# Performance work log

Hardware: AMD Instinct MI355X
Metric: run time of the kernel (lower is better)

Reference implementation:

```python
import jax, jax.numpy as jnp
import numpy as np


def setup_inputs() -> dict:
    key = jax.random.key(0)
    k1, k2 = jax.random.split(key)
    out = jax.random.uniform(k1, (32, 128, 128, 9, 5), dtype=jnp.float32)
    target = jax.random.uniform(k2, (32, 128, 128, 3, 6), dtype=jnp.float32)
    return {"out": out, "target": target}


def _loss(out, target):
    # out: [B, GX, GY, A, 5], target: [B, GX, GY, Q, 6]
    B, GX, GY, Q, _ = target.shape
    A = out.shape[3]
    # the original loop breaks after qub == 0, so only the first gt per cell is used
    st = target[:, :, :, 0, :]            # [B, GX, GY, 6]
    pos = st[..., 5] > 0.8                # [B, GX, GY] positive-cell mask

    dtype = out.dtype
    # grid-cell centers zxdwx / zxdwy
    zx = (jnp.arange(GX, dtype=dtype) / GX + 1.0 / (2 * GX))[None, :, None, None]
    zy = (jnp.arange(GY, dtype=dtype) / GY + 1.0 / (2 * GY))[None, None, :, None]

    # gt box (center format) -> corners; broadcast over anchor dim
    acx = st[..., 0][..., None]
    acy = st[..., 1][..., None]
    aw = st[..., 2][..., None]
    ah = st[..., 3][..., None]
    ax1, ay1, ax2, ay2 = acx - aw / 2, acy - ah / 2, acx + aw / 2, acy + ah / 2

    # predicted box: offsets decoded relative to grid cell
    bcx = out[..., 0] - 0.5 + zx
    bcy = out[..., 1] - 0.5 + zy
    bw = out[..., 2] - 0.5 + 1.0 / GX
    bh = out[..., 3] - 0.5 + 1.0 / GY
    bx1, by1, bx2, by2 = bcx - bw / 2, bcy - bh / 2, bcx + bw / 2, bcy + bh / 2

    # IoU (intersection zeroed when either overlap extent <= 0)
    iw = jnp.minimum(ax2, bx2) - jnp.maximum(ax1, bx1)
    ih = jnp.minimum(ay2, by2) - jnp.maximum(ay1, by1)
    cross = jnp.where((iw > 0) & (ih > 0), iw * ih, 0.0)
    area_a = (ax2 - ax1) * (ay2 - ay1)
    area_b = (bx2 - bx1) * (by2 - by1)
    union = area_a + area_b - cross
    iou = cross / (union + 1e-6)

    # DIoU term: center distance over bound-box diagonal
    d = jnp.sqrt(((bx1 + bx2) / 2 - (ax1 + ax2) / 2) ** 2
                 + ((by1 + by2) / 2 - (ay1 + ay2) / 2) ** 2)
    cx1 = jnp.minimum(ax1, bx1)
    cy1 = jnp.minimum(ay1, by1)
    cx2 = jnp.maximum(ax2, bx2)
    cy2 = jnp.maximum(ay2, by2)
    c = jnp.sqrt((cx2 - cx1) ** 2 + (cy2 - cy1) ** 2)
    diou = iou - d ** 2 / c ** 2

    # CIoU aspect-ratio term
    v = (4.0 / np.pi ** 2) * (jnp.arctan((ax2 - ax1) / (ay2 - ay1))
                              - jnp.arctan((bx2 - bx1) / (by2 - by1))) ** 2
    alpha = v / (1 - iou + v)
    los = 1 - (diou - alpha * v)      # [B, GX, GY, A]

    obj = out[..., 4]
    posA = pos[..., None]             # broadcast mask over anchors

    jsq = (jnp.sum(pos) * A).astype(dtype)
    qit = (jnp.sum(~pos) * A).astype(dtype)
    allloss = jnp.sum(jnp.where(posA, los + (1 - obj), 0.0))
    jbb = jnp.sum(jnp.where(posA, iou, 0.0))
    huhuh = jnp.sum(jnp.where(posA, 1 - obj, 0.0))
    zsd = jnp.sum(jnp.where(posA, (1 - obj) ** 2, obj ** 2))

    return (allloss / jsq + zsd / (jsq + qit), jbb / jsq, huhuh / jsq)


def reference(out, target):
    return _loss(out, target)
```

## Files before the change

kernel.cpp:

```cpp
#include <hip/hip_runtime.h>
#include <math.h>

constexpr int kGX     = 128;
constexpr int kGY     = 128;
constexpr int kA      = 9;
constexpr int kNCells = 32 * kGX * kGY;
constexpr int kN      = kNCells * kA;

constexpr int kGroups        = kN / 4;
constexpr int kTiles         = kGroups / 256;
constexpr int kTilesPerBlock = 2;
constexpr int kBlocks        = kTiles / kTilesPerBlock;
static_assert(kBlocks * kTilesPerBlock * 256 * 4 == kN, "exact cover");

__device__ inline float frcp(float x) { return __builtin_amdgcn_rcpf(x); }

__device__ inline float fast_atan(float r) {
    const float x = fabsf(r);
    const bool inv = x > 1.f;
    const float t = inv ? frcp(x) : x;
    const float t2 = t * t;
    float p = fmaf(t2, 0.0208351f, -0.0851330f);
    p = fmaf(t2, p, 0.1801410f);
    p = fmaf(t2, p, -0.3302995f);
    p = fmaf(t2, p, 0.9998660f);
    p = t * p;
    float res = inv ? (1.5707963f - p) : p;
    return r < 0.f ? -res : res;
}

struct Rec {
    float ax1, ax2, ay1, ay2, acx, acy, area, atg, zx, zy, posf;
};

__device__ inline Rec make_rec(const float* __restrict__ tgt, int cell) {
    const float2* t2p = (const float2*)(tgt + (size_t)cell * 18);
    const float2 a01 = t2p[0];
    const float2 a23 = t2p[1];
    const float conf = ((const float*)t2p)[5];
    Rec r;
    r.acx = a01.x; r.acy = a01.y;
    r.ax1 = a01.x - 0.5f * a23.x; r.ax2 = a01.x + 0.5f * a23.x;
    r.ay1 = a01.y - 0.5f * a23.y; r.ay2 = a01.y + 0.5f * a23.y;
    r.area = a23.x * a23.y;
    r.atg  = fast_atan(a23.x * frcp(a23.y));
    const int gy = cell & (kGY - 1);
    const int gx = (cell >> 7) & (kGX - 1);
    r.zx = (float)gx * (1.f / kGX) + 0.5f / kGX;
    r.zy = (float)gy * (1.f / kGY) + 0.5f / kGY;
    r.posf = (conf > 0.8f) ? 1.f : 0.f;
    return r;
}

__global__ __launch_bounds__(256)
void loss_main(const float* __restrict__ outp, const float* __restrict__ tgt,
               double* __restrict__ acc, int mode) {
    __shared__ float4 sbuf[1280];

    const int tid = threadIdx.x;
    float t_jsq = 0.f, t_all = 0.f, t_jbb = 0.f, t_huh = 0.f, t_zsd = 0.f;

    for (int tt = 0; tt < kTilesPerBlock; ++tt) {
        const int tile = blockIdx.x * kTilesPerBlock + tt;
        const int gid  = tile * 256 + tid;
        const int a0   = gid * 4;

        const int cell0 = (int)(__umulhi((unsigned)a0, 0x38E38E39u) >> 1);
        const int r0    = a0 - cell0 * 9;
        const int cell1 = min(cell0 + 1, kNCells - 1);
        const Rec RA = make_rec(tgt, cell0);
        const Rec RB = make_rec(tgt, cell1);

        if (tt) __syncthreads();
        const float4* src = (const float4*)outp + (size_t)tile * 1280;
        #pragma unroll
        for (int k = 0; k < 5; ++k) sbuf[k * 256 + tid] = src[k * 256 + tid];
        __syncthreads();

        const float* so = (const float*)sbuf + tid * 20;
        const float4 q0 = *(const float4*)(so +  0);
        const float4 q1 = *(const float4*)(so +  4);
        const float4 q2 = *(const float4*)(so +  8);
        const float4 q3 = *(const float4*)(so + 12);
        const float4 q4 = *(const float4*)(so + 16);

        const float o[20] = {q0.x, q0.y, q0.z, q0.w, q1.x, q1.y, q1.z, q1.w,
                             q2.x, q2.y, q2.z, q2.w, q3.x, q3.y, q3.z, q3.w,
                             q4.x, q4.y, q4.z, q4.w};

        #pragma unroll
        for (int j = 0; j < 4; ++j) {
            const bool cross = (r0 + j) >= 9;
            const float ax1 = cross ? RB.ax1 : RA.ax1, ax2 = cross ? RB.ax2 : RA.ax2;
            const float ay1 = cross ? RB.ay1 : RA.ay1, ay2 = cross ? RB.ay2 : RA.ay2;
            const float acx = cross ? RB.acx : RA.acx, acy = cross ? RB.acy : RA.acy;
            const float area_a = cross ? RB.area : RA.area;
            const float atan_a = cross ? RB.atg : RA.atg;
            const float zx = cross ? RB.zx : RA.zx, zy = cross ? RB.zy : RA.zy;
            const float posf = cross ? RB.posf : RA.posf;
            const bool pos = posf > 0.5f;

            const float o0 = o[j * 5 + 0], o1 = o[j * 5 + 1], o2 = o[j * 5 + 2];
            const float o3 = o[j * 5 + 3], obj = o[j * 5 + 4];

            const float bcx = o0 - 0.5f + zx;
            const float bcy = o1 - 0.5f + zy;
            const float bw  = o2 - 0.5f + (1.f / kGX);
            const float bh  = o3 - 0.5f + (1.f / kGY);
            const float bx1 = bcx - 0.5f * bw, bx2 = bcx + 0.5f * bw;
            const float by1 = bcy - 0.5f * bh, by2 = bcy + 0.5f * bh;

            const float iw = fminf(ax2, bx2) - fmaxf(ax1, bx1);
            const float ih = fminf(ay2, by2) - fmaxf(ay1, by1);
            const float cross_a = (iw > 0.f && ih > 0.f) ? iw * ih : 0.f;
            const float uni = area_a + bw * bh - cross_a;
            const float iou = cross_a * frcp(uni + 1e-6f);

            const float dx = bcx - acx, dy = bcy - acy;
            const float d2 = dx * dx + dy * dy;
            const float cw  = fmaxf(ax2, bx2) - fminf(ax1, bx1);
            const float chh = fmaxf(ay2, by2) - fminf(ay1, by1);
            const float c2 = cw * cw + chh * chh;
            const float diou = iou - d2 * frcp(c2);

            const float dat = atan_a - fast_atan(bw * frcp(bh));
            const float v = 0.4052847345693511f * dat * dat;
            const float alpha = v * frcp(1.f - iou + v);
            const float los = 1.f - (diou - alpha * v);
            const float om = 1.f - obj;

            t_jsq += posf;
            t_all += pos ? (los + om) : 0.f;
            t_jbb += pos ? iou : 0.f;
            t_huh += pos ? om : 0.f;
            t_zsd += pos ? om * om : obj * obj;
        }
    }

    const int lane = threadIdx.x & 63;
    const int wv   = threadIdx.x >> 6;
    float vals[5] = {t_jsq, t_all, t_jbb, t_huh, t_zsd};
    #pragma unroll
    for (int i = 0; i < 5; ++i) {
        float x = vals[i];
        #pragma unroll
        for (int off = 32; off > 0; off >>= 1) x += __shfl_down(x, off, 64);
        vals[i] = x;
    }
    __shared__ float smem[4][5];
    __syncthreads();
    if (lane == 0) {
        #pragma unroll
        for (int i = 0; i < 5; ++i) smem[wv][i] = vals[i];
    }
    __syncthreads();
    if (threadIdx.x < 5) {
        const double sv = (double)smem[0][threadIdx.x] + (double)smem[1][threadIdx.x] +
                          (double)smem[2][threadIdx.x] + (double)smem[3][threadIdx.x];
        if (mode) acc[(size_t)blockIdx.x * 5 + threadIdx.x] = sv;
        else atomicAdd(&acc[threadIdx.x], sv);
    }
}

__global__ __launch_bounds__(256)
void loss_final(const double* __restrict__ acc, float* __restrict__ res, int n_part) {
    if (n_part > 0) {
        double v[5] = {0, 0, 0, 0, 0};
        for (int j = threadIdx.x; j < n_part; j += 256) {
            #pragma unroll
            for (int i = 0; i < 5; ++i) v[i] += acc[(size_t)j * 5 + i];
        }
        #pragma unroll
        for (int i = 0; i < 5; ++i) {
            double x = v[i];
            #pragma unroll
            for (int off = 32; off > 0; off >>= 1) x += __shfl_down(x, off, 64);
            v[i] = x;
        }
        __shared__ double sm[4][5];
        const int lane = threadIdx.x & 63, wv = threadIdx.x >> 6;
        if (lane == 0) {
            #pragma unroll
            for (int i = 0; i < 5; ++i) sm[wv][i] = v[i];
        }
        __syncthreads();
        if (threadIdx.x == 0) {
            #pragma unroll
            for (int i = 0; i < 5; ++i) v[i] = sm[0][i] + sm[1][i] + sm[2][i] + sm[3][i];
            const double jsq = v[0], total = (double)kN;
            res[0] = (float)(v[1] / jsq + v[4] / total);
            res[1] = (float)(v[2] / jsq);
            res[2] = (float)(v[3] / jsq);
        }
    } else if (threadIdx.x == 0) {
        const double jsq = acc[0], total = (double)kN;
        res[0] = (float)(acc[1] / jsq + acc[4] / total);
        res[1] = (float)(acc[2] / jsq);
        res[2] = (float)(acc[3] / jsq);
    }
}

extern "C" void kernel_launch(void* const* d_in, const int* in_sizes, int n_in,
                              void* d_out, int out_size, void* d_ws, size_t ws_size,
                              hipStream_t stream) {
    const float* outp = (const float*)d_in[0];
    const float* tgt  = (const float*)d_in[1];
    float* res = (float*)d_out;
    double* acc = (double*)d_ws;

    const bool partials = ws_size >= (size_t)kBlocks * 5 * sizeof(double);
    if (!partials) hipMemsetAsync(acc, 0, 5 * sizeof(double), stream);
    loss_main<<<kBlocks, 256, 0, stream>>>(outp, tgt, acc, partials ? 1 : 0);
    loss_final<<<1, 256, 0, stream>>>(acc, res, partials ? kBlocks : 0);
}
```

Measured before the change: 172.5 us.

## Load anchor outputs directly into registers and process eight anchors per thread

```diff
diff --git a/kernel.cpp b/kernel.cpp
--- a/kernel.cpp
+++ b/kernel.cpp
@@ -7,11 +7,10 @@
 constexpr int kNCells = 32 * kGX * kGY;
 constexpr int kN      = kNCells * kA;
 
-constexpr int kGroups        = kN / 4;
-constexpr int kTiles         = kGroups / 256;
-constexpr int kTilesPerBlock = 2;
-constexpr int kBlocks        = kTiles / kTilesPerBlock;
-static_assert(kBlocks * kTilesPerBlock * 256 * 4 == kN, "exact cover");
+constexpr int kAnch   = 8;
+constexpr int kThreads= 256;
+constexpr int kBlocks = kN / (kThreads * kAnch);
+static_assert(kBlocks * kThreads * kAnch == kN, "exact cover");
 
 __device__ inline float frcp(float x) { return __builtin_amdgcn_rcpf(x); }
 
@@ -55,86 +54,74 @@
 __global__ __launch_bounds__(256)
 void loss_main(const float* __restrict__ outp, const float* __restrict__ tgt,
                double* __restrict__ acc, int mode) {
-    __shared__ float4 sbuf[1280];
-
-    const int tid = threadIdx.x;
+    const int gid = blockIdx.x * kThreads + threadIdx.x;
+    const int a0  = gid * kAnch;
+
+    const float4* o4 = (const float4*)outp + (size_t)gid * 10;
+    const float4 q0 = o4[0], q1 = o4[1], q2 = o4[2], q3 = o4[3], q4 = o4[4];
+    const float4 q5 = o4[5], q6 = o4[6], q7 = o4[7], q8 = o4[8], q9 = o4[9];
+
+    const int cell0 = (int)(__umulhi((unsigned)a0, 0x38E38E39u) >> 1);
+    const int r0    = a0 - cell0 * 9;
+    const int cell1 = min(cell0 + 1, kNCells - 1);
+
+    const Rec RA = make_rec(tgt, cell0);
+    const Rec RB = make_rec(tgt, cell1);
+
+    const float o[40] = {q0.x, q0.y, q0.z, q0.w, q1.x, q1.y, q1.z, q1.w,
+                         q2.x, q2.y, q2.z, q2.w, q3.x, q3.y, q3.z, q3.w,
+                         q4.x, q4.y, q4.z, q4.w, q5.x, q5.y, q5.z, q5.w,
+                         q6.x, q6.y, q6.z, q6.w, q7.x, q7.y, q7.z, q7.w,
+                         q8.x, q8.y, q8.z, q8.w, q9.x, q9.y, q9.z, q9.w};
+
     float t_jsq = 0.f, t_all = 0.f, t_jbb = 0.f, t_huh = 0.f, t_zsd = 0.f;
 
-    for (int tt = 0; tt < kTilesPerBlock; ++tt) {
-        const int tile = blockIdx.x * kTilesPerBlock + tt;
-        const int gid  = tile * 256 + tid;
-        const int a0   = gid * 4;
-
-        const int cell0 = (int)(__umulhi((unsigned)a0, 0x38E38E39u) >> 1);
-        const int r0    = a0 - cell0 * 9;
-        const int cell1 = min(cell0 + 1, kNCells - 1);
-        const Rec RA = make_rec(tgt, cell0);
-        const Rec RB = make_rec(tgt, cell1);
-
-        if (tt) __syncthreads();
-        const float4* src = (const float4*)outp + (size_t)tile * 1280;
-        #pragma unroll
-        for (int k = 0; k < 5; ++k) sbuf[k * 256 + tid] = src[k * 256 + tid];
-        __syncthreads();
-
-        const float* so = (const float*)sbuf + tid * 20;
-        const float4 q0 = *(const float4*)(so +  0);
-        const float4 q1 = *(const float4*)(so +  4);
-        const float4 q2 = *(const float4*)(so +  8);
-        const float4 q3 = *(const float4*)(so + 12);
-        const float4 q4 = *(const float4*)(so + 16);
-
-        const float o[20] = {q0.x, q0.y, q0.z, q0.w, q1.x, q1.y, q1.z, q1.w,
-                             q2.x, q2.y, q2.z, q2.w, q3.x, q3.y, q3.z, q3.w,
-                             q4.x, q4.y, q4.z, q4.w};
-
-        #pragma unroll
-        for (int j = 0; j < 4; ++j) {
-            const bool cross = (r0 + j) >= 9;
-            const float ax1 = cross ? RB.ax1 : RA.ax1, ax2 = cross ? RB.ax2 : RA.ax2;
-            const float ay1 = cross ? RB.ay1 : RA.ay1, ay2 = cross ? RB.ay2 : RA.ay2;
-            const float acx = cross ? RB.acx : RA.acx, acy = cross ? RB.acy : RA.acy;
-            const float area_a = cross ? RB.area : RA.area;
-            const float atan_a = cross ? RB.atg : RA.atg;
-            const float zx = cross ? RB.zx : RA.zx, zy = cross ? RB.zy : RA.zy;
-            const float posf = cross ? RB.posf : RA.posf;
-            const bool pos = posf > 0.5f;
-
-            const float o0 = o[j * 5 + 0], o1 = o[j * 5 + 1], o2 = o[j * 5 + 2];
-            const float o3 = o[j * 5 + 3], obj = o[j * 5 + 4];
-
-            const float bcx = o0 - 0.5f + zx;
-            const float bcy = o1 - 0.5f + zy;
-            const float bw  = o2 - 0.5f + (1.f / kGX);
-            const float bh  = o3 - 0.5f + (1.f / kGY);
-            const float bx1 = bcx - 0.5f * bw, bx2 = bcx + 0.5f * bw;
-            const float by1 = bcy - 0.5f * bh, by2 = bcy + 0.5f * bh;
-
-            const float iw = fminf(ax2, bx2) - fmaxf(ax1, bx1);
-            const float ih = fminf(ay2, by2) - fmaxf(ay1, by1);
-            const float cross_a = (iw > 0.f && ih > 0.f) ? iw * ih : 0.f;
-            const float uni = area_a + bw * bh - cross_a;
-            const float iou = cross_a * frcp(uni + 1e-6f);
-
-            const float dx = bcx - acx, dy = bcy - acy;
-            const float d2 = dx * dx + dy * dy;
-            const float cw  = fmaxf(ax2, bx2) - fminf(ax1, bx1);
-            const float chh = fmaxf(ay2, by2) - fminf(ay1, by1);
-            const float c2 = cw * cw + chh * chh;
-            const float diou = iou - d2 * frcp(c2);
-
-            const float dat = atan_a - fast_atan(bw * frcp(bh));
-            const float v = 0.4052847345693511f * dat * dat;
-            const float alpha = v * frcp(1.f - iou + v);
-            const float los = 1.f - (diou - alpha * v);
-            const float om = 1.f - obj;
-
-            t_jsq += posf;
-            t_all += pos ? (los + om) : 0.f;
-            t_jbb += pos ? iou : 0.f;
-            t_huh += pos ? om : 0.f;
-            t_zsd += pos ? om * om : obj * obj;
-        }
+    #pragma unroll
+    for (int j = 0; j < kAnch; ++j) {
+        const bool cross = (r0 + j) >= 9;
+        const float ax1 = cross ? RB.ax1 : RA.ax1, ax2 = cross ? RB.ax2 : RA.ax2;
+        const float ay1 = cross ? RB.ay1 : RA.ay1, ay2 = cross ? RB.ay2 : RA.ay2;
+        const float acx = cross ? RB.acx : RA.acx, acy = cross ? RB.acy : RA.acy;
+        const float area_a = cross ? RB.area : RA.area;
+        const float atan_a = cross ? RB.atg : RA.atg;
+        const float zx = cross ? RB.zx : RA.zx, zy = cross ? RB.zy : RA.zy;
+        const float posf = cross ? RB.posf : RA.posf;
+        const bool pos = posf > 0.5f;
+
+        const float o0 = o[j * 5 + 0], o1 = o[j * 5 + 1], o2 = o[j * 5 + 2];
+        const float o3 = o[j * 5 + 3], obj = o[j * 5 + 4];
+
+        const float bcx = o0 - 0.5f + zx;
+        const float bcy = o1 - 0.5f + zy;
+        const float bw  = o2 - 0.5f + (1.f / kGX);
+        const float bh  = o3 - 0.5f + (1.f / kGY);
+        const float bx1 = bcx - 0.5f * bw, bx2 = bcx + 0.5f * bw;
+        const float by1 = bcy - 0.5f * bh, by2 = bcy + 0.5f * bh;
+
+        const float iw = fminf(ax2, bx2) - fmaxf(ax1, bx1);
+        const float ih = fminf(ay2, by2) - fmaxf(ay1, by1);
+        const float cross_a = (iw > 0.f && ih > 0.f) ? iw * ih : 0.f;
+        const float uni = area_a + bw * bh - cross_a;
+        const float iou = cross_a * frcp(uni + 1e-6f);
+
+        const float dx = bcx - acx, dy = bcy - acy;
+        const float d2 = dx * dx + dy * dy;
+        const float cw  = fmaxf(ax2, bx2) - fminf(ax1, bx1);
+        const float chh = fmaxf(ay2, by2) - fminf(ay1, by1);
+        const float c2 = cw * cw + chh * chh;
+        const float diou = iou - d2 * frcp(c2);
+
+        const float dat = atan_a - fast_atan(bw * frcp(bh));
+        const float v = 0.4052847345693511f * dat * dat;
+        const float alpha = v * frcp(1.f - iou + v);
+        const float los = 1.f - (diou - alpha * v);
+        const float om = 1.f - obj;
+
+        t_jsq += posf;
+        t_all += pos ? (los + om) : 0.f;
+        t_jbb += pos ? iou : 0.f;
+        t_huh += pos ? om : 0.f;
+        t_zsd += pos ? om * om : obj * obj;
     }
 
     const int lane = threadIdx.x & 63;
@@ -148,7 +135,6 @@
         vals[i] = x;
     }
     __shared__ float smem[4][5];
-    __syncthreads();
     if (lane == 0) {
         #pragma unroll
         for (int i = 0; i < 5; ++i) smem[wv][i] = vals[i];
@@ -210,6 +196,6 @@
 
     const bool partials = ws_size >= (size_t)kBlocks * 5 * sizeof(double);
     if (!partials) hipMemsetAsync(acc, 0, 5 * sizeof(double), stream);
-    loss_main<<<kBlocks, 256, 0, stream>>>(outp, tgt, acc, partials ? 1 : 0);
+    loss_main<<<kBlocks, kThreads, 0, stream>>>(outp, tgt, acc, partials ? 1 : 0);
     loss_final<<<1, 256, 0, stream>>>(acc, res, partials ? kBlocks : 0);
 }
```

New measurement: 173.6 us. No clear change (+0.6%).
